# Optimization experiments

Hardware: AMD Instinct MI355X
Metric: run time of the kernel (lower is better)

## Reference

```python
import jax, jax.numpy as jnp
import numpy as np

T, B, H, E, V, L = 256, 32, 1024, 1024, 32000, 2


def lstm_stack(x, h0, c0, Wih, Whh, bih, bhh):
    # x: [T,B,E]; Wih/Whh: [L,4H,H]; bih/bhh: [L,4H]; h0/c0: [L,B,H]
    for l in range(Wih.shape[0]):
        Wi, Wh, bi, bh = Wih[l], Whh[l], bih[l], bhh[l]

        def step(carry, xt, Wi=Wi, Wh=Wh, bi=bi, bh=bh):
            h, c = carry
            g = xt @ Wi.T + h @ Wh.T + bi + bh  # [B,4H]
            i_, f_, g_, o_ = jnp.split(g, 4, axis=-1)  # PyTorch gate order i,f,g,o
            c = jax.nn.sigmoid(f_) * c + jax.nn.sigmoid(i_) * jnp.tanh(g_)
            h = jax.nn.sigmoid(o_) * jnp.tanh(c)
            return (h, c), h

        (_, _), x = jax.lax.scan(step, (h0[l], c0[l]), x)
    return x  # [T,B,H]


def setup_inputs() -> dict:
    key = jax.random.key(0)
    ks = jax.random.split(key, 20)
    u = lambda k, s: jax.random.uniform(k, s, jnp.float32, -0.1, 0.1)
    n = lambda k, s: 0.02 * jax.random.normal(k, s, jnp.float32)
    return {
        'data_left': jax.random.randint(ks[0], (T, B), 0, V),
        'data_right': jax.random.randint(ks[1], (T, B), 0, V),
        'h0_left': jnp.zeros((L, B, H), jnp.float32),
        'c0_left': jnp.zeros((L, B, H), jnp.float32),
        'h0_right': jnp.zeros((L, B, H), jnp.float32),
        'c0_right': jnp.zeros((L, B, H), jnp.float32),
        'emb': u(ks[2], (V, E)),
        'Wih_l': n(ks[3], (L, 4 * H, H)), 'Whh_l': n(ks[4], (L, 4 * H, H)),
        'bih_l': n(ks[5], (L, 4 * H)), 'bhh_l': n(ks[6], (L, 4 * H)),
        'Wih_r': n(ks[7], (L, 4 * H, H)), 'Whh_r': n(ks[8], (L, 4 * H, H)),
        'bih_r': n(ks[9], (L, 4 * H)), 'bhh_r': n(ks[10], (L, 4 * H)),
        'attn_w': n(ks[11], (1, 3 * H)), 'attn_b': n(ks[12], (1,)),
        'trans_w': n(ks[13], (H, 3 * H)), 'trans_b': n(ks[14], (H,)),
        'dec_w': u(ks[15], (V, H)), 'dec_b': jnp.zeros((V,), jnp.float32),
    }


def reference(data_left, data_right, h0_left, c0_left, h0_right, c0_right,
              emb, Wih_l, Whh_l, bih_l, bhh_l, Wih_r, Whh_r, bih_r, bhh_r,
              attn_w, attn_b, trans_w, trans_b, dec_w, dec_b):
    # Encode (dropout=0 -> identity). Right branch runs on the flipped sequence.
    xL = emb[data_left]                    # [T,B,E]
    xR = emb[data_right[::-1]]             # [T,B,E]
    outL = lstm_stack(xL, h0_left, c0_left, Wih_l, Whh_l, bih_l, bhh_l)   # [T,B,H]
    outR = lstm_stack(xR, h0_right, c0_right, Wih_r, Whh_r, bih_r, bhh_r)[::-1]

    # attn Linear(3H,1) splits into per-chunk projections: [left_i, right_i, ctx_k]
    w1, w2, w3 = jnp.split(attn_w[0], 3)   # each [H]
    a = outL @ w1 + outR @ w2 + attn_b[0]  # [T,B] query-dependent part
    sL = outL @ w3                          # [T,B]
    sR = outR @ w3                          # [T,B]

    # context for query i has fixed length T+1: k<=i -> outL[k], k>i -> outR[k-1]
    kk = jnp.arange(T + 1)
    ii = jnp.arange(T)
    maskL = kk[None, :] <= ii[:, None]      # [T,T+1]
    sL_pad = jnp.concatenate([sL, jnp.zeros((1, B), sL.dtype)], 0)   # [T+1,B]
    sR_sh = jnp.concatenate([jnp.zeros((1, B), sR.dtype), sR], 0)    # sR[k-1]
    ctx_s = jnp.where(maskL[:, :, None], sL_pad[None], sR_sh[None])  # [T,T+1,B]
    scores = jnp.tanh(a[:, None, :] + ctx_s)                          # [T,T+1,B]
    p = jax.nn.softmax(scores, axis=1)

    pL = p * maskL[:, :, None]
    pR = p * (~maskL)[:, :, None]
    # context_vector[i] = sum_k p[i,k] * ctx[i,k]
    cv = (jnp.einsum('ikb,kbh->ibh', pL[:, :T], outL)
          + jnp.einsum('ikb,kbh->ibh', pR[:, 1:], outR))              # [T,B,H]

    h3 = jnp.concatenate([outL, outR, cv], axis=-1)                   # [T,B,3H]
    pred = jnp.tanh(h3 @ trans_w.T + trans_b)                         # [T,B,H]
    decoded = pred @ dec_w.T + dec_b                                  # [T,B,V]
    return decoded
```

## Files before the change

kernel.cpp:

```cpp
#include <hip/hip_runtime.h>
#include <hip/hip_bf16.h>


using bf16 = __hip_bfloat16;
typedef __attribute__((ext_vector_type(8))) __bf16 bf16x8;
typedef __attribute__((ext_vector_type(4))) float f32x4;
typedef __attribute__((ext_vector_type(4))) short short4v;

#define T_ 256
#define B_ 32
#define H_ 1024
#define V_ 32000

__device__ __forceinline__ float b2f(bf16 x) { return __bfloat162float(x); }
__device__ __forceinline__ bf16 f2b(float x) { return __float2bfloat16(x); }
__device__ __forceinline__ float us2f(unsigned short u) {
  union { unsigned u; float f; } w; w.u = ((unsigned)u) << 16; return w.f;
}
__device__ __forceinline__ void st4(bf16* dst, float4 f) {
  union { bf16 h[4]; short4v s; } u;
  u.h[0] = f2b(f.x); u.h[1] = f2b(f.y); u.h[2] = f2b(f.z); u.h[3] = f2b(f.w);
  *reinterpret_cast<short4v*>(dst) = u.s;
}
__device__ __forceinline__ bf16x8 cvt8(float4 a, float4 b) {
  union { bf16 h[8]; bf16x8 v; } u;
  u.h[0] = f2b(a.x); u.h[1] = f2b(a.y); u.h[2] = f2b(a.z); u.h[3] = f2b(a.w);
  u.h[4] = f2b(b.x); u.h[5] = f2b(b.y); u.h[6] = f2b(b.z); u.h[7] = f2b(b.w);
  return u.v;
}
__device__ __forceinline__ void gload_lds16(const bf16* g, bf16* l) {
  __builtin_amdgcn_global_load_lds(
      (const __attribute__((address_space(1))) void*)g,
      (__attribute__((address_space(3))) void*)l, 16, 0, 0);
}

__global__ __launch_bounds__(256)
void cvt_f32_bf16(const float* __restrict__ src, bf16* __restrict__ dst, long n)
{
  long i = ((long)blockIdx.x * 256 + threadIdx.x) * 8;
  if (i >= n) return;
  float4 a = *reinterpret_cast<const float4*>(src + i);
  float4 b = *reinterpret_cast<const float4*>(src + i + 4);
  st4(dst + i, a); st4(dst + i + 4, b);
}

__global__ __launch_bounds__(128)
void embed_gather(const int* __restrict__ dl, const int* __restrict__ dr,
                  const float* __restrict__ emb,
                  bf16* __restrict__ xL, bf16* __restrict__ xR)
{
  int wg = blockIdx.x;
  int d  = wg >> 13;
  int r  = wg & 8191;
  int t  = r >> 5, b = r & 31;
  int tok = d ? dr[(T_ - 1 - t) * B_ + b] : dl[r];
  const float* src = emb + (long)tok * H_;
  bf16* dst = (d ? xR : xL) + (long)r * H_;
  int e = threadIdx.x * 8;
  float4 a = *reinterpret_cast<const float4*>(src + e);
  float4 c = *reinterpret_cast<const float4*>(src + e + 4);
  st4(dst + e, a); st4(dst + e + 4, c);
}

#define LSTRIDE 40

template<int ACT, int HASBIAS, int OUTF32>
__global__ __launch_bounds__(256)
void gemm_bt(const bf16* __restrict__ A, const float* __restrict__ Bwf,
             const float* __restrict__ bias, void* __restrict__ Cv,
             int M, int N, int K)
{
  __shared__ __align__(16) bf16 As[128 * LSTRIDE];
  __shared__ __align__(16) bf16 Bs[128 * LSTRIDE];
  const int tid  = threadIdx.x;
  const int lane = tid & 63;
  const int wave = tid >> 6;
  const int wm = wave >> 1, wn = wave & 1;
  const long bm = blockIdx.x, bn = blockIdx.y;

  const bf16*  Ag = A + bm * 128 * (long)K;
  const float* Bg = Bwf + bn * 128 * (long)K;

  f32x4 acc[4][4] = {};

  const int nk = K >> 5;
  for (int kt = 0; kt < nk; ++kt) {
    const int k0 = kt * 32;
    __syncthreads();
    #pragma unroll
    for (int j = 0; j < 2; ++j) {
      int chunk = j * 256 + tid;
      int row = chunk >> 2, c4 = chunk & 3;
      *reinterpret_cast<bf16x8*>(&As[row * LSTRIDE + c4 * 8]) =
          *reinterpret_cast<const bf16x8*>(&Ag[(long)row * K + k0 + c4 * 8]);
    }
    #pragma unroll
    for (int j = 0; j < 4; ++j) {
      int chunk = j * 256 + tid;
      int row = chunk >> 3, c4f = chunk & 7;
      float4 f = *reinterpret_cast<const float4*>(&Bg[(long)row * K + k0 + c4f * 4]);
      st4(&Bs[row * LSTRIDE + c4f * 4], f);
    }
    __syncthreads();
    bf16x8 af[4], bfr[4];
    #pragma unroll
    for (int m = 0; m < 4; ++m)
      af[m] = *reinterpret_cast<const bf16x8*>(
          &As[(wm * 64 + m * 16 + (lane & 15)) * LSTRIDE + (lane >> 4) * 8]);
    #pragma unroll
    for (int n = 0; n < 4; ++n)
      bfr[n] = *reinterpret_cast<const bf16x8*>(
          &Bs[(wn * 64 + n * 16 + (lane & 15)) * LSTRIDE + (lane >> 4) * 8]);
    #pragma unroll
    for (int m = 0; m < 4; ++m)
      #pragma unroll
      for (int n = 0; n < 4; ++n)
        acc[m][n] = __builtin_amdgcn_mfma_f32_16x16x32_bf16(af[m], bfr[n], acc[m][n], 0, 0, 0);
  }

  #pragma unroll
  for (int m = 0; m < 4; ++m) {
    int row = (int)bm * 128 + wm * 64 + m * 16 + ((lane >> 4) << 2);
    #pragma unroll
    for (int n = 0; n < 4; ++n) {
      int col = (int)bn * 128 + wn * 64 + n * 16 + (lane & 15);
      float bv = HASBIAS ? bias[col] : 0.f;
      #pragma unroll
      for (int j = 0; j < 4; ++j) {
        float v = acc[m][n][j] + bv;
        if (ACT) v = tanhf(v);
        long off = (long)(row + j) * N + col;
        if (OUTF32) reinterpret_cast<float*>(Cv)[off] = v;
        else        reinterpret_cast<bf16*>(Cv)[off] = f2b(v);
      }
    }
  }
}

template<int ACT, int HASBIAS, int OUTF32>
__global__ __launch_bounds__(256)
void gemm_bb(const bf16* __restrict__ A, const bf16* __restrict__ Bw,
             const float* __restrict__ bias, void* __restrict__ Cv,
             int M, int N, int K)
{
  __shared__ __align__(16) bf16 As[128 * 32];
  __shared__ __align__(16) bf16 Bs[128 * 32];
  const int tid  = threadIdx.x;
  const int lane = tid & 63;
  const int wave = tid >> 6;
  const int wm = wave >> 1, wn = wave & 1;
  const long bm = blockIdx.x, bn = blockIdx.y;

  const bf16* Ag = A  + bm * 128 * (long)K;
  const bf16* Bg = Bw + bn * 128 * (long)K;

  const int r0  = tid >> 2;
  const int cgd = (tid & 3) ^ (r0 & 3);
  const int rsw = ((lane >> 4) ^ (lane & 3)) * 8;

  f32x4 acc[4][4] = {};
  const int nk = K >> 5;
  for (int kt = 0; kt < nk; ++kt) {
    const int k0 = kt * 32;
    __syncthreads();
    #pragma unroll
    for (int j = 0; j < 2; ++j) {
      int row = j * 64 + r0;
      gload_lds16(Ag + (long)row * K + k0 + cgd * 8, As + (j * 256 + wave * 64) * 8);
      gload_lds16(Bg + (long)row * K + k0 + cgd * 8, Bs + (j * 256 + wave * 64) * 8);
    }
    __syncthreads();
    bf16x8 af[4], bfr[4];
    #pragma unroll
    for (int m = 0; m < 4; ++m)
      af[m] = *reinterpret_cast<const bf16x8*>(
          &As[(wm * 64 + m * 16 + (lane & 15)) * 32 + rsw]);
    #pragma unroll
    for (int n = 0; n < 4; ++n)
      bfr[n] = *reinterpret_cast<const bf16x8*>(
          &Bs[(wn * 64 + n * 16 + (lane & 15)) * 32 + rsw]);
    #pragma unroll
    for (int m = 0; m < 4; ++m)
      #pragma unroll
      for (int n = 0; n < 4; ++n)
        acc[m][n] = __builtin_amdgcn_mfma_f32_16x16x32_bf16(af[m], bfr[n], acc[m][n], 0, 0, 0);
  }

  #pragma unroll
  for (int m = 0; m < 4; ++m) {
    int row = (int)bm * 128 + wm * 64 + m * 16 + ((lane >> 4) << 2);
    #pragma unroll
    for (int n = 0; n < 4; ++n) {
      int col = (int)bn * 128 + wn * 64 + n * 16 + (lane & 15);
      float bv = HASBIAS ? bias[col] : 0.f;
      #pragma unroll
      for (int j = 0; j < 4; ++j) {
        float v = acc[m][n][j] + bv;
        if (ACT) v = tanhf(v);
        long off = (long)(row + j) * N + col;
        if (OUTF32) reinterpret_cast<float*>(Cv)[off] = v;
        else        reinterpret_cast<bf16*>(Cv)[off] = f2b(v);
      }
    }
  }
}

__global__ __launch_bounds__(256, 1)
void lstm_layer(const bf16* __restrict__ WhhL, const bf16* __restrict__ WhhR,
                const bf16* __restrict__ giL,  const bf16* __restrict__ giR,
                const float* __restrict__ bihL, const float* __restrict__ bhhL,
                const float* __restrict__ bihR, const float* __restrict__ bhhR,
                const float* __restrict__ h0L, const float* __restrict__ h0R,
                const float* __restrict__ c0L, const float* __restrict__ c0R,
                bf16* __restrict__ houtL, bf16* __restrict__ houtR,
                int revR, unsigned* __restrict__ bar)
{
  const int d    = blockIdx.y;
  const int u0   = blockIdx.x * 16;
  const int tid  = threadIdx.x;
  const int lane = tid & 63;
  const int wq   = tid >> 6;
  const long BH  = (long)B_ * H_;

  const bf16*  Whh = d ? WhhR : WhhL;
  const bf16*  gi0 = d ? giR  : giL;
  const float* bi  = d ? bihR : bihL;
  const float* bh  = d ? bhhR : bhhL;
  const float* h0  = d ? h0R  : h0L;
  const float* c0  = d ? c0R  : c0L;
  bf16* hout       = d ? houtR : houtL;
  const int rev    = d ? revR : 0;
  unsigned* cnt    = bar + d;

  (void)__hip_atomic_load(cnt, __ATOMIC_ACQUIRE, __HIP_MEMORY_SCOPE_AGENT);

  const int klo = (lane >> 4) * 8;

  bf16x8 w_reg[4][8];
  #pragma unroll
  for (int g = 0; g < 4; ++g) {
    const bf16* p = Whh + ((long)g * H_ + u0 + (lane & 15)) * H_ + wq * 256 + klo;
    #pragma unroll
    for (int q = 0; q < 8; ++q)
      w_reg[g][q] = *reinterpret_cast<const bf16x8*>(p + q * 32);
  }

  const int b  = tid >> 3;
  const int u  = (tid & 7) * 2;
  const int ug = u0 + u;

  float bsum[4][2];
  #pragma unroll
  for (int g = 0; g < 4; ++g) {
    bsum[g][0] = bi[g * H_ + ug]     + bh[g * H_ + ug];
    bsum[g][1] = bi[g * H_ + ug + 1] + bh[g * H_ + ug + 1];
  }
  float cc0 = c0[(long)b * H_ + ug];
  float cc1 = c0[(long)b * H_ + ug + 1];

  __shared__ float gbuf[4][4][32][16];

  for (int s = 0; s < T_; ++s) {
    unsigned giv[4];
    {
      const bf16* gis = gi0 + (long)s * (B_ * 4 * H_) + (long)b * (4 * H_);
      #pragma unroll
      for (int g = 0; g < 4; ++g)
        giv[g] = *reinterpret_cast<const unsigned*>(&gis[g * H_ + ug]);
    }

    f32x4 acc[4][2];
    #pragma unroll
    for (int g = 0; g < 4; ++g) {
      acc[g][0] = f32x4{0.f, 0.f, 0.f, 0.f};
      acc[g][1] = f32x4{0.f, 0.f, 0.f, 0.f};
    }

    if (s == 0) {
      const float* ap0 = h0 + (long)(lane & 15) * H_ + wq * 256 + klo;
      const float* ap1 = ap0 + 16L * H_;
      #pragma unroll
      for (int q = 0; q < 8; ++q) {
        bf16x8 a0 = cvt8(*reinterpret_cast<const float4*>(ap0 + q * 32),
                         *reinterpret_cast<const float4*>(ap0 + q * 32 + 4));
        bf16x8 a1 = cvt8(*reinterpret_cast<const float4*>(ap1 + q * 32),
                         *reinterpret_cast<const float4*>(ap1 + q * 32 + 4));
        #pragma unroll
        for (int g = 0; g < 4; ++g) {
          acc[g][0] = __builtin_amdgcn_mfma_f32_16x16x32_bf16(a0, w_reg[g][q], acc[g][0], 0, 0, 0);
          acc[g][1] = __builtin_amdgcn_mfma_f32_16x16x32_bf16(a1, w_reg[g][q], acc[g][1], 0, 0, 0);
        }
      }
    } else {
      const bf16* hp  = hout + (long)(rev ? (T_ - s) : (s - 1)) * BH;
      const bf16* ap0 = hp + (long)(lane & 15) * H_ + wq * 256 + klo;
      const bf16* ap1 = ap0 + 16L * H_;
      #pragma unroll
      for (int q = 0; q < 8; ++q) {
        bf16x8 a0 = *reinterpret_cast<const bf16x8*>(ap0 + q * 32);
        bf16x8 a1 = *reinterpret_cast<const bf16x8*>(ap1 + q * 32);
        #pragma unroll
        for (int g = 0; g < 4; ++g) {
          acc[g][0] = __builtin_amdgcn_mfma_f32_16x16x32_bf16(a0, w_reg[g][q], acc[g][0], 0, 0, 0);
          acc[g][1] = __builtin_amdgcn_mfma_f32_16x16x32_bf16(a1, w_reg[g][q], acc[g][1], 0, 0, 0);
        }
      }
    }

    {
      int cr = (lane >> 4) << 2, ccu = lane & 15;
      #pragma unroll
      for (int g = 0; g < 4; ++g)
        #pragma unroll
        for (int j = 0; j < 4; ++j) {
          gbuf[wq][g][cr + j][ccu]      = acc[g][0][j];
          gbuf[wq][g][16 + cr + j][ccu] = acc[g][1][j];
        }
    }
    __syncthreads();

    {
      float g4[4][2];
      #pragma unroll
      for (int g = 0; g < 4; ++g) {
        float p0 = gbuf[0][g][b][u]     + gbuf[1][g][b][u];
        float p1 = gbuf[2][g][b][u]     + gbuf[3][g][b][u];
        float q0 = gbuf[0][g][b][u + 1] + gbuf[1][g][b][u + 1];
        float q1 = gbuf[2][g][b][u + 1] + gbuf[3][g][b][u + 1];
        g4[g][0] = (p0 + p1) + us2f((unsigned short)(giv[g] & 0xffffu)) + bsum[g][0];
        g4[g][1] = (q0 + q1) + us2f((unsigned short)(giv[g] >> 16))     + bsum[g][1];
      }
      float si0 = 1.f / (1.f + expf(-g4[0][0])), si1 = 1.f / (1.f + expf(-g4[0][1]));
      float sf0 = 1.f / (1.f + expf(-g4[1][0])), sf1 = 1.f / (1.f + expf(-g4[1][1]));
      float tg0 = tanhf(g4[2][0]),               tg1 = tanhf(g4[2][1]);
      float so0 = 1.f / (1.f + expf(-g4[3][0])), so1 = 1.f / (1.f + expf(-g4[3][1]));
      cc0 = sf0 * cc0 + si0 * tg0;
      cc1 = sf1 * cc1 + si1 * tg1;
      float hn0 = so0 * tanhf(cc0);
      float hn1 = so1 * tanhf(cc1);
      union { bf16 h[2]; unsigned w; } up;
      up.h[0] = f2b(hn0); up.h[1] = f2b(hn1);
      long wIdx = rev ? (long)(T_ - 1 - s) : (long)s;
      __hip_atomic_store(
          reinterpret_cast<unsigned*>(&hout[wIdx * BH + (long)b * H_ + ug]),
          up.w, __ATOMIC_RELAXED, __HIP_MEMORY_SCOPE_AGENT);
    }

    if (s + 1 < T_) {
      __syncthreads();
      if (tid == 0) {
        __hip_atomic_fetch_add(cnt, 1u, __ATOMIC_RELAXED, __HIP_MEMORY_SCOPE_AGENT);
        unsigned tgt = 64u * (unsigned)(s + 1);
        while (__hip_atomic_load(cnt, __ATOMIC_RELAXED, __HIP_MEMORY_SCOPE_AGENT) < tgt)
          __builtin_amdgcn_s_sleep(2);
      }
      __syncthreads();
    }
  }
}

__global__ __launch_bounds__(256)
void attn_scores(const bf16* __restrict__ outL, const bf16* __restrict__ outR,
                 const float* __restrict__ attn_w, const float* __restrict__ attn_b,
                 float* __restrict__ a, float* __restrict__ sL, float* __restrict__ sR)
{
  int r = blockIdx.x;
  int tid = threadIdx.x;
  const bf16* oL = outL + (long)r * H_;
  const bf16* oR = outR + (long)r * H_;
  int e = tid * 4;
  float pa = 0.f, pl = 0.f, pr = 0.f;
  #pragma unroll
  for (int j = 0; j < 4; ++j) {
    float l_ = b2f(oL[e + j]), r_ = b2f(oR[e + j]);
    float w1 = attn_w[e + j];
    float w2 = attn_w[H_ + e + j];
    float w3 = attn_w[2 * H_ + e + j];
    pa += w1 * l_ + w2 * r_;
    pl += w3 * l_;
    pr += w3 * r_;
  }
  #pragma unroll
  for (int off = 32; off > 0; off >>= 1) {
    pa += __shfl_down(pa, off);
    pl += __shfl_down(pl, off);
    pr += __shfl_down(pr, off);
  }
  __shared__ float red[3][4];
  int wave = tid >> 6, lane = tid & 63;
  if (lane == 0) { red[0][wave] = pa; red[1][wave] = pl; red[2][wave] = pr; }
  __syncthreads();
  if (tid == 0) {
    a[r]  = red[0][0] + red[0][1] + red[0][2] + red[0][3] + attn_b[0];
    sL[r] = red[1][0] + red[1][1] + red[1][2] + red[1][3];
    sR[r] = red[2][0] + red[2][1] + red[2][2] + red[2][3];
  }
}

__global__ __launch_bounds__(64)
void attn_softmax(const float* __restrict__ a, const float* __restrict__ sL,
                  const float* __restrict__ sR, float* __restrict__ p)
{
  int i = blockIdx.x, b = blockIdx.y;
  int lane = threadIdx.x;
  float av = a[i * B_ + b];
  float sc[5];
  float mx = -1e30f;
  #pragma unroll
  for (int q = 0; q < 5; ++q) {
    int k = lane + q * 64;
    float v = -1e30f;
    if (k < 257) {
      float ctx = (k <= i) ? sL[k * B_ + b] : sR[(k - 1) * B_ + b];
      v = tanhf(av + ctx);
    }
    sc[q] = v;
    mx = fmaxf(mx, v);
  }
  #pragma unroll
  for (int off = 32; off > 0; off >>= 1) mx = fmaxf(mx, __shfl_xor(mx, off));
  float sum = 0.f;
  #pragma unroll
  for (int q = 0; q < 5; ++q) {
    int k = lane + q * 64;
    float e = (k < 257) ? __expf(sc[q] - mx) : 0.f;
    sc[q] = e; sum += e;
  }
  #pragma unroll
  for (int off = 32; off > 0; off >>= 1) sum += __shfl_xor(sum, off);
  float inv = 1.f / sum;
  long base = ((long)b * T_ + i) * 257;
  #pragma unroll
  for (int q = 0; q < 5; ++q) {
    int k = lane + q * 64;
    if (k < 257) p[base + k] = sc[q] * inv;
  }
}

__global__ __launch_bounds__(256)
void h3_copy(const bf16* __restrict__ outL, const bf16* __restrict__ outR,
             bf16* __restrict__ h3)
{
  long gid = (long)blockIdx.x * 256 + threadIdx.x;
  long e = gid * 8;
  if (e >= (long)T_ * B_ * H_) return;
  long r = e >> 10; int h = (int)(e & 1023);
  *reinterpret_cast<bf16x8*>(&h3[r * 3 * H_ + h]) =
      *reinterpret_cast<const bf16x8*>(&outL[e]);
  *reinterpret_cast<bf16x8*>(&h3[r * 3 * H_ + H_ + h]) =
      *reinterpret_cast<const bf16x8*>(&outR[e]);
}

__global__ __launch_bounds__(256)
void attn_cv(const float* __restrict__ p, const bf16* __restrict__ outL,
             const bf16* __restrict__ outR, bf16* __restrict__ h3)
{
  int b = blockIdx.y;
  int i0 = blockIdx.x * 16;
  int tid = threadIdx.x;
  __shared__ float ps[16][257];
  for (int idx = tid; idx < 16 * 257; idx += 256) {
    int ii = idx / 257, k = idx % 257;
    ps[ii][k] = p[((long)b * T_ + i0 + ii) * 257 + k];
  }
  __syncthreads();
  float acc[16][4] = {};
  int h0 = tid * 4;
  for (int k = 0; k < 257; ++k) {
    float vL[4] = {0.f, 0.f, 0.f, 0.f}, vR[4] = {0.f, 0.f, 0.f, 0.f};
    if (k < 256) {
      short4v v = *reinterpret_cast<const short4v*>(&outL[((long)k * B_ + b) * H_ + h0]);
      vL[0] = us2f((unsigned short)v[0]); vL[1] = us2f((unsigned short)v[1]);
      vL[2] = us2f((unsigned short)v[2]); vL[3] = us2f((unsigned short)v[3]);
    }
    if (k >= 1) {
      short4v v = *reinterpret_cast<const short4v*>(&outR[((long)(k - 1) * B_ + b) * H_ + h0]);
      vR[0] = us2f((unsigned short)v[0]); vR[1] = us2f((unsigned short)v[1]);
      vR[2] = us2f((unsigned short)v[2]); vR[3] = us2f((unsigned short)v[3]);
    }
    #pragma unroll
    for (int ii = 0; ii < 16; ++ii) {
      float pv = ps[ii][k];
      bool useL = (i0 + ii) >= k;
      #pragma unroll
      for (int j = 0; j < 4; ++j)
        acc[ii][j] += pv * (useL ? vL[j] : vR[j]);
    }
  }
  #pragma unroll
  for (int ii = 0; ii < 16; ++ii)
    #pragma unroll
    for (int j = 0; j < 4; ++j)
      h3[((long)(i0 + ii) * B_ + b) * 3 * H_ + 2 * H_ + h0 + j] = f2b(acc[ii][j]);
}

extern "C" void kernel_launch(void* const* d_in, const int* in_sizes, int n_in,
                              void* d_out, int out_size, void* d_ws, size_t ws_size,
                              hipStream_t stream)
{
  (void)in_sizes; (void)n_in; (void)out_size;
  const int*   data_left  = (const int*)  d_in[0];
  const int*   data_right = (const int*)  d_in[1];
  const float* h0_left    = (const float*)d_in[2];
  const float* c0_left    = (const float*)d_in[3];
  const float* h0_right   = (const float*)d_in[4];
  const float* c0_right   = (const float*)d_in[5];
  const float* emb        = (const float*)d_in[6];
  const float* Wih_l      = (const float*)d_in[7];
  const float* Whh_l      = (const float*)d_in[8];
  const float* bih_l      = (const float*)d_in[9];
  const float* bhh_l      = (const float*)d_in[10];
  const float* Wih_r      = (const float*)d_in[11];
  const float* Whh_r      = (const float*)d_in[12];
  const float* bih_r      = (const float*)d_in[13];
  const float* bhh_r      = (const float*)d_in[14];
  const float* attn_w     = (const float*)d_in[15];
  const float* attn_b     = (const float*)d_in[16];
  const float* trans_w    = (const float*)d_in[17];
  const float* trans_b    = (const float*)d_in[18];
  const float* dec_w      = (const float*)d_in[19];
  const float* dec_b      = (const float*)d_in[20];

  char* ws = (char*)d_ws;
  bf16*     XL   = (bf16*)    (ws + 0L);
  bf16*     XR   = (bf16*)    (ws + 16777216L);
  bf16*     GI_L = (bf16*)    (ws + 33554432L);
  bf16*     GI_R = (bf16*)    (ws + 100663296L);
  bf16*     H0L  = (bf16*)    (ws + 167772160L);
  bf16*     H0R  = (bf16*)    (ws + 184549376L);
  unsigned* BAR  = (unsigned*)(ws + 201326592L);
  bf16*     WHHB = (bf16*)    (ws + 201588736L);
  bf16*     WIHB   = (bf16*)  (ws + 235143168L);
  bf16*     TRANSB = (bf16*)  (ws + 268697600L);
  bf16*     DECB   = (bf16*)  (ws + 274989056L);
  const bool fast = ws_size >= 340525056UL;
  bf16*  O1L  = XL;
  bf16*  O1R  = XR;
  bf16*  H3   = GI_L;
  float* P_   = (float*)(ws + 100663296L);
  float* A_   = (float*)(ws + 109084672L);
  float* SL_  = (float*)(ws + 109117440L);
  float* SR_  = (float*)(ws + 109150208L);
  bf16*  PRED = (bf16*) (ws + 109182976L);

  const long BH  = (long)B_ * H_;
  const long WL  = 4L * H_ * H_;
  bf16* WHHB_l = WHHB;
  bf16* WHHB_r = WHHB + 2 * WL;
  bf16* WIHB_l = WIHB;
  bf16* WIHB_r = WIHB + 2 * WL;

  cvt_f32_bf16<<<4096, 256, 0, stream>>>(Whh_l, WHHB_l, 2 * WL);
  cvt_f32_bf16<<<4096, 256, 0, stream>>>(Whh_r, WHHB_r, 2 * WL);
  if (fast) {
    cvt_f32_bf16<<<4096, 256, 0, stream>>>(Wih_l, WIHB_l, 2 * WL);
    cvt_f32_bf16<<<4096, 256, 0, stream>>>(Wih_r, WIHB_r, 2 * WL);
    cvt_f32_bf16<<<1536, 256, 0, stream>>>(trans_w, TRANSB, (long)H_ * 3 * H_);
    cvt_f32_bf16<<<16000, 256, 0, stream>>>(dec_w, DECB, (long)V_ * H_);
  }

  embed_gather<<<16384, 128, 0, stream>>>(data_left, data_right, emb, XL, XR);

  if (fast) {
    gemm_bb<0,0,0><<<dim3(64, 32), 256, 0, stream>>>(XL, WIHB_l, nullptr, GI_L, 8192, 4096, 1024);
    gemm_bb<0,0,0><<<dim3(64, 32), 256, 0, stream>>>(XR, WIHB_r, nullptr, GI_R, 8192, 4096, 1024);
  } else {
    gemm_bt<0,0,0><<<dim3(64, 32), 256, 0, stream>>>(XL, Wih_l, nullptr, GI_L, 8192, 4096, 1024);
    gemm_bt<0,0,0><<<dim3(64, 32), 256, 0, stream>>>(XR, Wih_r, nullptr, GI_R, 8192, 4096, 1024);
  }

  hipMemsetAsync(BAR, 0, 256, stream);
  lstm_layer<<<dim3(64, 2), 256, 0, stream>>>(
      WHHB_l, WHHB_r, GI_L, GI_R,
      bih_l, bhh_l, bih_r, bhh_r,
      h0_left, h0_right, c0_left, c0_right,
      H0L, H0R, 0, BAR);

  if (fast) {
    gemm_bb<0,0,0><<<dim3(64, 32), 256, 0, stream>>>(H0L, WIHB_l + WL, nullptr, GI_L, 8192, 4096, 1024);
    gemm_bb<0,0,0><<<dim3(64, 32), 256, 0, stream>>>(H0R, WIHB_r + WL, nullptr, GI_R, 8192, 4096, 1024);
  } else {
    gemm_bt<0,0,0><<<dim3(64, 32), 256, 0, stream>>>(H0L, Wih_l + WL, nullptr, GI_L, 8192, 4096, 1024);
    gemm_bt<0,0,0><<<dim3(64, 32), 256, 0, stream>>>(H0R, Wih_r + WL, nullptr, GI_R, 8192, 4096, 1024);
  }

  hipMemsetAsync(BAR, 0, 256, stream);
  lstm_layer<<<dim3(64, 2), 256, 0, stream>>>(
      WHHB_l + WL, WHHB_r + WL, GI_L, GI_R,
      bih_l + 4 * H_, bhh_l + 4 * H_, bih_r + 4 * H_, bhh_r + 4 * H_,
      h0_left + BH, h0_right + BH, c0_left + BH, c0_right + BH,
      O1L, O1R, 1, BAR);

  attn_scores<<<8192, 256, 0, stream>>>(O1L, O1R, attn_w, attn_b, A_, SL_, SR_);
  attn_softmax<<<dim3(256, 32), 64, 0, stream>>>(A_, SL_, SR_, P_);
  h3_copy<<<4096, 256, 0, stream>>>(O1L, O1R, H3);
  attn_cv<<<dim3(16, 32), 256, 0, stream>>>(P_, O1L, O1R, H3);

  if (fast) {
    gemm_bb<1,1,0><<<dim3(64, 8),   256, 0, stream>>>(H3,   TRANSB, trans_b, PRED, 8192, 1024, 3072);
    gemm_bb<0,1,1><<<dim3(64, 250), 256, 0, stream>>>(PRED, DECB,   dec_b,   d_out, 8192, 32000, 1024);
  } else {
    gemm_bt<1,1,0><<<dim3(64, 8),   256, 0, stream>>>(H3,   trans_w, trans_b, PRED, 8192, 1024, 3072);
    gemm_bt<0,1,1><<<dim3(64, 250), 256, 0, stream>>>(PRED, dec_w,   dec_b,   d_out, 8192, 32000, 1024);
  }
}
```

Before: 4.461 ms.

## Replace bf16 GEMM with 256x256-tile double-buffered 8-wave kernel

Swaps the 128x128, single-buffered, 4-wave bf16 MFMA GEMM for a 256x256-tile kernel with 8 waves and a K-step of 64. LDS is double-buffered with XOR-swizzled global-to-LDS loads, so the next tile prefetches while the current one computes. It also adds an XCD-aware block-index swizzle and s_setprio around the MFMA bursts. The aim is higher arithmetic intensity and hidden load latency for the input-projection, transform and decoder GEMMs. In exchange it uses 128KB of LDS and one block per CU, and the grid sizes must now divide exactly into tiles and by 8.

```diff
diff --git a/kernel.cpp b/kernel.cpp
--- a/kernel.cpp
+++ b/kernel.cpp
@@ -138,66 +138,110 @@
 }
 
 template<int ACT, int HASBIAS, int OUTF32>
-__global__ __launch_bounds__(256)
-void gemm_bb(const bf16* __restrict__ A, const bf16* __restrict__ Bw,
-             const float* __restrict__ bias, void* __restrict__ Cv,
-             int M, int N, int K)
-{
-  __shared__ __align__(16) bf16 As[128 * 32];
-  __shared__ __align__(16) bf16 Bs[128 * 32];
+__global__ __launch_bounds__(512, 1)
+void gemm8(const bf16* __restrict__ A, const bf16* __restrict__ Bw,
+           const float* __restrict__ bias, void* __restrict__ Cv,
+           int M, int N, int K, int mt)
+{
+  __shared__ __align__(16) bf16 As[2][256 * 64];
+  __shared__ __align__(16) bf16 Bs[2][256 * 64];
   const int tid  = threadIdx.x;
   const int lane = tid & 63;
   const int wave = tid >> 6;
-  const int wm = wave >> 1, wn = wave & 1;
-  const long bm = blockIdx.x, bn = blockIdx.y;
-
-  const bf16* Ag = A  + bm * 128 * (long)K;
-  const bf16* Bg = Bw + bn * 128 * (long)K;
-
-  const int r0  = tid >> 2;
-  const int cgd = (tid & 3) ^ (r0 & 3);
-  const int rsw = ((lane >> 4) ^ (lane & 3)) * 8;
-
-  f32x4 acc[4][4] = {};
-  const int nk = K >> 5;
-  for (int kt = 0; kt < nk; ++kt) {
-    const int k0 = kt * 32;
-    __syncthreads();
-    #pragma unroll
-    for (int j = 0; j < 2; ++j) {
-      int row = j * 64 + r0;
-      gload_lds16(Ag + (long)row * K + k0 + cgd * 8, As + (j * 256 + wave * 64) * 8);
-      gload_lds16(Bg + (long)row * K + k0 + cgd * 8, Bs + (j * 256 + wave * 64) * 8);
-    }
-    __syncthreads();
-    bf16x8 af[4], bfr[4];
-    #pragma unroll
-    for (int m = 0; m < 4; ++m)
-      af[m] = *reinterpret_cast<const bf16x8*>(
-          &As[(wm * 64 + m * 16 + (lane & 15)) * 32 + rsw]);
-    #pragma unroll
-    for (int n = 0; n < 4; ++n)
-      bfr[n] = *reinterpret_cast<const bf16x8*>(
-          &Bs[(wn * 64 + n * 16 + (lane & 15)) * 32 + rsw]);
-    #pragma unroll
-    for (int m = 0; m < 4; ++m)
-      #pragma unroll
-      for (int n = 0; n < 4; ++n)
-        acc[m][n] = __builtin_amdgcn_mfma_f32_16x16x32_bf16(af[m], bfr[n], acc[m][n], 0, 0, 0);
-  }
-
-  #pragma unroll
-  for (int m = 0; m < 4; ++m) {
-    int row = (int)bm * 128 + wm * 64 + m * 16 + ((lane >> 4) << 2);
-    #pragma unroll
-    for (int n = 0; n < 4; ++n) {
-      int col = (int)bn * 128 + wn * 64 + n * 16 + (lane & 15);
+  const int wm = wave >> 2, wn = wave & 3;
+
+  const int nwg = (int)gridDim.x;
+  const int cpx = nwg >> 3;
+  const int bid = (int)blockIdx.x;
+  const int swz = (bid & 7) * cpx + (bid >> 3);
+  const long bm = swz % mt, bn = swz / mt;
+
+  const bf16* Ag = A  + bm * 256 * (long)K;
+  const bf16* Bg = Bw + bn * 256 * (long)K;
+
+  f32x4 acc[8][4] = {};
+  const int nt = K >> 6;
+
+  auto stage = [&](int buf, int kt) {
+    const int k0 = kt * 64;
+    #pragma unroll
+    for (int g = 0; g < 8; ++g) {
+      const int gl = g & 3;
+      const int c  = gl * 512 + tid;
+      const int r  = c >> 3;
+      const int sl = (c & 7) ^ (r & 7);
+      if (g < 4)
+        gload_lds16(Ag + (long)r * K + k0 + sl * 8, &As[buf][gl * 4096 + wave * 512]);
+      else
+        gload_lds16(Bg + (long)r * K + k0 + sl * 8, &Bs[buf][gl * 4096 + wave * 512]);
+    }
+  };
+
+  stage(0, 0);
+  asm volatile("s_waitcnt vmcnt(0)" ::: "memory");
+  __builtin_amdgcn_s_barrier();
+
+  for (int j = 0; j < nt; ++j) {
+    const int cur = j & 1, nxt = cur ^ 1;
+    if (j + 1 < nt) {
+      stage(nxt, j + 1);
+      asm volatile("s_waitcnt vmcnt(8)" ::: "memory");
+    } else {
+      asm volatile("s_waitcnt vmcnt(0)" ::: "memory");
+    }
+    __builtin_amdgcn_s_barrier();
+
+    bf16x8 bfr[4][2];
+    #pragma unroll
+    for (int fn = 0; fn < 4; ++fn)
+      #pragma unroll
+      for (int kk = 0; kk < 2; ++kk) {
+        int rb = wn * 64 + fn * 16 + (lane & 15);
+        int u  = (lane >> 4) + 4 * kk;
+        bfr[fn][kk] = *reinterpret_cast<const bf16x8*>(
+            &Bs[cur][rb * 64 + (u ^ (rb & 7)) * 8]);
+      }
+
+    #pragma unroll
+    for (int p = 0; p < 4; ++p) {
+      bf16x8 afr[2][2];
+      #pragma unroll
+      for (int q = 0; q < 2; ++q)
+        #pragma unroll
+        for (int kk = 0; kk < 2; ++kk) {
+          int ra = wm * 128 + (p * 2 + q) * 16 + (lane & 15);
+          int u  = (lane >> 4) + 4 * kk;
+          afr[q][kk] = *reinterpret_cast<const bf16x8*>(
+              &As[cur][ra * 64 + (u ^ (ra & 7)) * 8]);
+        }
+      __builtin_amdgcn_s_barrier();
+      __builtin_amdgcn_s_setprio(1);
+      #pragma unroll
+      for (int q = 0; q < 2; ++q)
+        #pragma unroll
+        for (int fn = 0; fn < 4; ++fn) {
+          acc[p * 2 + q][fn] = __builtin_amdgcn_mfma_f32_16x16x32_bf16(
+              afr[q][0], bfr[fn][0], acc[p * 2 + q][fn], 0, 0, 0);
+          acc[p * 2 + q][fn] = __builtin_amdgcn_mfma_f32_16x16x32_bf16(
+              afr[q][1], bfr[fn][1], acc[p * 2 + q][fn], 0, 0, 0);
+        }
+      __builtin_amdgcn_s_setprio(0);
+      __builtin_amdgcn_s_barrier();
+    }
+  }
+
+  #pragma unroll
+  for (int fm = 0; fm < 8; ++fm) {
+    int row = (int)bm * 256 + wm * 128 + fm * 16 + ((lane >> 4) << 2);
+    #pragma unroll
+    for (int fn = 0; fn < 4; ++fn) {
+      int col = (int)bn * 256 + wn * 64 + fn * 16 + (lane & 15);
       float bv = HASBIAS ? bias[col] : 0.f;
       #pragma unroll
-      for (int j = 0; j < 4; ++j) {
-        float v = acc[m][n][j] + bv;
+      for (int jj = 0; jj < 4; ++jj) {
+        float v = acc[fm][fn][jj] + bv;
         if (ACT) v = tanhf(v);
-        long off = (long)(row + j) * N + col;
+        long off = (long)(row + jj) * N + col;
         if (OUTF32) reinterpret_cast<float*>(Cv)[off] = v;
         else        reinterpret_cast<bf16*>(Cv)[off] = f2b(v);
       }
@@ -562,8 +606,8 @@
   embed_gather<<<16384, 128, 0, stream>>>(data_left, data_right, emb, XL, XR);
 
   if (fast) {
-    gemm_bb<0,0,0><<<dim3(64, 32), 256, 0, stream>>>(XL, WIHB_l, nullptr, GI_L, 8192, 4096, 1024);
-    gemm_bb<0,0,0><<<dim3(64, 32), 256, 0, stream>>>(XR, WIHB_r, nullptr, GI_R, 8192, 4096, 1024);
+    gemm8<0,0,0><<<512, 512, 0, stream>>>(XL, WIHB_l, nullptr, GI_L, 8192, 4096, 1024, 32);
+    gemm8<0,0,0><<<512, 512, 0, stream>>>(XR, WIHB_r, nullptr, GI_R, 8192, 4096, 1024, 32);
   } else {
     gemm_bt<0,0,0><<<dim3(64, 32), 256, 0, stream>>>(XL, Wih_l, nullptr, GI_L, 8192, 4096, 1024);
     gemm_bt<0,0,0><<<dim3(64, 32), 256, 0, stream>>>(XR, Wih_r, nullptr, GI_R, 8192, 4096, 1024);
@@ -577,8 +621,8 @@
       H0L, H0R, 0, BAR);
 
   if (fast) {
-    gemm_bb<0,0,0><<<dim3(64, 32), 256, 0, stream>>>(H0L, WIHB_l + WL, nullptr, GI_L, 8192, 4096, 1024);
-    gemm_bb<0,0,0><<<dim3(64, 32), 256, 0, stream>>>(H0R, WIHB_r + WL, nullptr, GI_R, 8192, 4096, 1024);
+    gemm8<0,0,0><<<512, 512, 0, stream>>>(H0L, WIHB_l + WL, nullptr, GI_L, 8192, 4096, 1024, 32);
+    gemm8<0,0,0><<<512, 512, 0, stream>>>(H0R, WIHB_r + WL, nullptr, GI_R, 8192, 4096, 1024, 32);
   } else {
     gemm_bt<0,0,0><<<dim3(64, 32), 256, 0, stream>>>(H0L, Wih_l + WL, nullptr, GI_L, 8192, 4096, 1024);
     gemm_bt<0,0,0><<<dim3(64, 32), 256, 0, stream>>>(H0R, Wih_r + WL, nullptr, GI_R, 8192, 4096, 1024);
@@ -597,8 +641,8 @@
   attn_cv<<<dim3(16, 32), 256, 0, stream>>>(P_, O1L, O1R, H3);
 
   if (fast) {
-    gemm_bb<1,1,0><<<dim3(64, 8),   256, 0, stream>>>(H3,   TRANSB, trans_b, PRED, 8192, 1024, 3072);
-    gemm_bb<0,1,1><<<dim3(64, 250), 256, 0, stream>>>(PRED, DECB,   dec_b,   d_out, 8192, 32000, 1024);
+    gemm8<1,1,0><<<128, 512, 0, stream>>>(H3, TRANSB, trans_b, PRED, 8192, 1024, 3072, 32);
+    gemm8<0,1,1><<<4000, 512, 0, stream>>>(PRED, DECB, dec_b, d_out, 8192, 32000, 1024, 32);
   } else {
     gemm_bt<1,1,0><<<dim3(64, 8),   256, 0, stream>>>(H3,   trans_w, trans_b, PRED, 8192, 1024, 3072);
     gemm_bt<0,1,1><<<dim3(64, 250), 256, 0, stream>>>(PRED, dec_w,   dec_b,   d_out, 8192, 32000, 1024);
```

Result: slower. 4.589 ms (+2.9%).
